# Kernel optimization log

Hardware: AMD Instinct MI355X
Metric: run time of the kernel (lower is better)

The kernel has to match this reference:

```python
import jax, jax.numpy as jnp
import numpy as np


def _laplacian_kernel(x, z, bandwidth):
    x_sq = jnp.sum(x * x, axis=-1, keepdims=True)          # [N, 1]
    z_sq = jnp.sum(z * z, axis=-1)[None, :]                # [1, M]
    d2 = x_sq + z_sq - 2.0 * jnp.einsum('nd,md->nm', x, z)  # [N, M]
    d = jnp.sqrt(jnp.maximum(d2, 0.0))
    return jnp.exp(-d / bandwidth)


def setup_inputs() -> dict:
    key = jax.random.key(0)
    k1, k2, k3 = jax.random.split(key, 3)
    N, M, D, Y = 8192, 20000, 1024, 256
    batch = jax.random.normal(k1, (N, D), dtype=jnp.float32)
    centers = jax.random.normal(k2, (M, D), dtype=jnp.float32)
    weight = jax.random.normal(k3, (M, Y), dtype=jnp.float32) * 0.02
    return {"batch": batch, "centers": centers, "weight": weight, "bandwidth": 10}


def reference(batch, centers, weight, bandwidth):
    kmat = _laplacian_kernel(batch, centers, float(bandwidth))  # [N, M]
    pred = kmat @ weight                                        # [N, Y]
    return pred
```

## Files before the change

### kernel.cpp

```cpp
#include <hip/hip_runtime.h>
#include <stdint.h>

#define N_ROWS 8192
#define D_DIM  1024
#define M_CENT 20000
#define M_PAD  20224
#define M_TILES 79
#define Y_DIM  256
#define BM 64
#define BN 256
#define BK 64
#define NCHUNK 16
#define MSPLIT 8
#define TILES_PER_SPLIT 10
#define LDSP_STRIDE 264

#define BUFE 20480
#define ZOFF 4096
#define POFF 20480

typedef __attribute__((ext_vector_type(4))) float  f32x4;
typedef __attribute__((ext_vector_type(8))) __bf16 bf16x8;

__device__ __forceinline__ unsigned short f2bf(float f) {
    union { float f; unsigned u; } v; v.f = f;
    unsigned u = v.u;
    u += 0x7FFFu + ((u >> 16) & 1u);
    return (unsigned short)(u >> 16);
}

__device__ __forceinline__ void gll16(void* lds, const void* g) {
    __builtin_amdgcn_global_load_lds(
        (const __attribute__((address_space(1))) void*)g,
        (__attribute__((address_space(3))) void*)lds, 16, 0, 0);
}

__global__ void cast_rows_kernel(const float* __restrict__ src,
                                 unsigned short* __restrict__ dst,
                                 float* __restrict__ sq, int nrows_valid) {
    int row = blockIdx.x;
    int t = threadIdx.x;
    float s = 0.f;
    if (row < nrows_valid) {
        float4 v = ((const float4*)(src + (size_t)row * D_DIM))[t];
        s = v.x * v.x + v.y * v.y + v.z * v.z + v.w * v.w;
        ushort4 o;
        o.x = f2bf(v.x); o.y = f2bf(v.y); o.z = f2bf(v.z); o.w = f2bf(v.w);
        ((ushort4*)(dst + (size_t)row * D_DIM))[t] = o;
    } else {
        ((ushort4*)(dst + (size_t)row * D_DIM))[t] = make_ushort4(0, 0, 0, 0);
    }
    __shared__ float red[4];
    for (int off = 32; off; off >>= 1) s += __shfl_down(s, off, 64);
    if ((t & 63) == 0) red[t >> 6] = s;
    __syncthreads();
    if (t == 0) sq[row] = red[0] + red[1] + red[2] + red[3];
}

__global__ void cast_wT_kernel(const float* __restrict__ w,
                               unsigned short* __restrict__ wT) {
    __shared__ float tile[32][33];
    int k0 = blockIdx.x * 32;
    int y0 = blockIdx.y * 32;
    int tx = threadIdx.x & 31;
    int ty = threadIdx.x >> 5;
    #pragma unroll
    for (int i = 0; i < 4; ++i) {
        int k = k0 + ty + i * 8;
        float v = (k < M_CENT) ? w[(size_t)k * Y_DIM + y0 + tx] : 0.f;
        tile[tx][ty + i * 8] = v;
    }
    __syncthreads();
    #pragma unroll
    for (int i = 0; i < 4; ++i) {
        int yl = ty + i * 8;
        wT[(size_t)(y0 + yl) * M_PAD + k0 + tx] = f2bf(tile[yl][tx]);
    }
}


#define STAGE(PAR, M0, KBASE) do {                                            \
    _Pragma("unroll")                                                         \
    for (int i_ = 0; i_ < 2; ++i_) {                   \
        int lin_ = t + i_ * 256;                                              \
        int row_ = lin_ >> 3, c_ = lin_ & 7;                                  \
        gll16(&lds_all[(PAR) * BUFE + lin_ * 8],                              \
              Xb + (size_t)(row0 + row_) * D_DIM + (KBASE) +                  \
                  ((c_ ^ (row_ & 7)) * 8));                                   \
    }                                                                         \
    _Pragma("unroll")                                                         \
    for (int i_ = 0; i_ < 8; ++i_) {                  \
        int lin_ = t + i_ * 256;                                              \
        int row_ = lin_ >> 3, c_ = lin_ & 7;                                  \
        gll16(&lds_all[(PAR) * BUFE + ZOFF + lin_ * 8],                       \
              Zb + (size_t)((M0) + row_) * D_DIM + (KBASE) +                  \
                  ((c_ ^ (row_ & 7)) * 8));                                   \
    } } while (0)

#define CHUNK(PAR, M0N, KBN) do {                                             \
    asm volatile("" ::: "memory");                                            \
    __builtin_amdgcn_s_barrier();                  \
    asm volatile("" ::: "memory");                                            \
    STAGE(PAR ^ 1, M0N, KBN);                                                 \
    __builtin_amdgcn_sched_barrier(0);                                        \
    asm volatile("s_waitcnt vmcnt(10)" ::: "memory");     \
    __builtin_amdgcn_s_barrier();            \
    asm volatile("" ::: "memory");                                            \
    _Pragma("unroll")                                                         \
    for (int kt_ = 0; kt_ < 2; ++kt_) {                                       \
        const int sw_ = ((kt_ * 4 + quad) ^ cx) * 8;                          \
        bf16x8 a_[4], b_[4];                                                  \
        _Pragma("unroll")                                                     \
        for (int it_ = 0; it_ < 4; ++it_)                                     \
            a_[it_] = *(const bf16x8*)&lds_all[(PAR) * BUFE +                 \
                (it_ * 16 + l16) * BK + sw_];                                 \
        _Pragma("unroll")                                                     \
        for (int jt_ = 0; jt_ < 4; ++jt_)                                     \
            b_[jt_] = *(const bf16x8*)&lds_all[(PAR) * BUFE + ZOFF +          \
                (wave * 64 + jt_ * 16 + l16) * BK + sw_];                     \
        __builtin_amdgcn_s_setprio(1);                                        \
        _Pragma("unroll")                                                     \
        for (int it_ = 0; it_ < 4; ++it_)                                     \
            _Pragma("unroll")                                                 \
            for (int jt_ = 0; jt_ < 4; ++jt_)                                 \
                S[it_ * 4 + jt_] = __builtin_amdgcn_mfma_f32_16x16x32_bf16(   \
                    a_[it_], b_[jt_], S[it_ * 4 + jt_], 0, 0, 0);             \
        __builtin_amdgcn_s_setprio(0);                                        \
    } } while (0)

__global__ void __launch_bounds__(256, 2)
fused_kernel(const unsigned short* __restrict__ Xb,
             const unsigned short* __restrict__ Zb,
             const unsigned short* __restrict__ WbT,
             const float* __restrict__ xsq,
             const float* __restrict__ zsq,
             const int* __restrict__ bwp,
             float* __restrict__ out) {
    __shared__ unsigned short lds_all[2 * BUFE];

    const int t    = threadIdx.x;
    const int wave = t >> 6;
    const int lane = t & 63;
    const int quad = lane >> 4;
    const int l16  = lane & 15;
    const int cx   = l16 & 7;

    const int row0 = blockIdx.x * BM;
    const int mt0  = blockIdx.y * TILES_PER_SPLIT;
    int mt_end = mt0 + TILES_PER_SPLIT;
    if (mt_end > M_TILES) mt_end = M_TILES;

    int bwi = *bwp;
    float bw;
    if (bwi > 0 && bwi < 1000000) bw = (float)bwi;
    else { union { int i; float f; } u; u.i = bwi; bw = u.f; }
    const float inv_bw = 1.0f / bw;

    const f32x4 vzero = {0.f, 0.f, 0.f, 0.f};
    f32x4 Oacc[16];
    #pragma unroll
    for (int i = 0; i < 16; ++i) Oacc[i] = vzero;

    STAGE(0, mt0 * BN, 0);
    __builtin_amdgcn_sched_barrier(0);

    for (int mt = mt0; mt < mt_end; ++mt) {
        const int m0 = mt * BN;
        const int m0next = (mt + 1 < mt_end) ? m0 + BN : m0;

        f32x4 S[16];
        #pragma unroll
        for (int i = 0; i < 16; ++i) S[i] = vzero;

        #pragma unroll 1
        for (int kc = 0; kc < NCHUNK; kc += 2) {
            const bool last = (kc + 2 == NCHUNK);
            CHUNK(0, m0, (kc + 1) * BK);
            CHUNK(1, last ? m0next : m0, last ? 0 : (kc + 2) * BK);
        }

        asm volatile("" ::: "memory");
        __builtin_amdgcn_s_barrier();
        asm volatile("" ::: "memory");

        f32x4 xq[4];
        #pragma unroll
        for (int it = 0; it < 4; ++it)
            xq[it] = *(const f32x4*)(xsq + row0 + it * 16 + quad * 4);
        float zq[4];
        #pragma unroll
        for (int jt = 0; jt < 4; ++jt)
            zq[jt] = zsq[m0 + wave * 64 + jt * 16 + l16];

        #pragma unroll
        for (int it = 0; it < 4; ++it) {
            #pragma unroll
            for (int jt = 0; jt < 4; ++jt) {
                f32x4 s4 = S[it * 4 + jt];
                const int col = wave * 64 + jt * 16 + l16;
                #pragma unroll
                for (int r = 0; r < 4; ++r) {
                    const int row = it * 16 + quad * 4 + r;
                    float d2 = xq[it][r] + zq[jt] - 2.0f * s4[r];
                    d2 = fmaxf(d2, 0.f);
                    float d;
                    asm("v_sqrt_f32 %0, %1" : "=v"(d) : "v"(d2));
                    float p = __expf(-d * inv_bw);
                    lds_all[POFF + row * LDSP_STRIDE + col] = f2bf(p);
                }
            }
        }
        asm volatile("s_waitcnt lgkmcnt(0)" ::: "memory");
        __builtin_amdgcn_s_barrier();
        asm volatile("" ::: "memory");

        #pragma unroll
        for (int ks = 0; ks < 8; ++ks) {
            const int koff = ks * 32 + quad * 8;
            bf16x8 a[4], b[4];
            #pragma unroll
            for (int rt = 0; rt < 4; ++rt)
                a[rt] = *(const bf16x8*)&lds_all[POFF +
                    (rt * 16 + l16) * LDSP_STRIDE + koff];
            #pragma unroll
            for (int ct = 0; ct < 4; ++ct) {
                const int y = wave * 64 + ct * 16 + l16;
                b[ct] = *(const bf16x8*)(WbT + (size_t)y * M_PAD + m0 + koff);
            }
            __builtin_amdgcn_s_setprio(1);
            #pragma unroll
            for (int rt = 0; rt < 4; ++rt)
                #pragma unroll
                for (int ct = 0; ct < 4; ++ct)
                    Oacc[rt * 4 + ct] = __builtin_amdgcn_mfma_f32_16x16x32_bf16(
                        a[rt], b[ct], Oacc[rt * 4 + ct], 0, 0, 0);
            __builtin_amdgcn_s_setprio(0);
        }
    }

    asm volatile("s_waitcnt vmcnt(0)" ::: "memory");

    #pragma unroll
    for (int rt = 0; rt < 4; ++rt) {
        #pragma unroll
        for (int ct = 0; ct < 4; ++ct) {
            f32x4 v = Oacc[rt * 4 + ct];
            const int y = wave * 64 + ct * 16 + l16;
            #pragma unroll
            for (int r = 0; r < 4; ++r) {
                const int row = row0 + rt * 16 + quad * 4 + r;
                atomicAdd(&out[(size_t)row * Y_DIM + y], v[r]);
            }
        }
    }
}

extern "C" void kernel_launch(void* const* d_in, const int* in_sizes, int n_in,
                              void* d_out, int out_size, void* d_ws, size_t ws_size,
                              hipStream_t stream) {
    const float* X = (const float*)d_in[0];
    const float* Z = (const float*)d_in[1];
    const float* W = (const float*)d_in[2];
    const int*  bw = (const int*)d_in[3];
    float* out = (float*)d_out;

    char* ws = (char*)d_ws;
    size_t off = 0;
    unsigned short* Xb  = (unsigned short*)(ws + off); off += (size_t)N_ROWS * D_DIM * 2;
    unsigned short* Zb  = (unsigned short*)(ws + off); off += (size_t)M_PAD * D_DIM * 2;
    unsigned short* WbT = (unsigned short*)(ws + off); off += (size_t)Y_DIM * M_PAD * 2;
    float* xsq = (float*)(ws + off); off += (size_t)N_ROWS * 4;
    float* zsq = (float*)(ws + off); off += (size_t)M_PAD * 4;

    hipMemsetAsync(d_out, 0, (size_t)out_size * sizeof(float), stream);
    cast_rows_kernel<<<N_ROWS, 256, 0, stream>>>(X, Xb, xsq, N_ROWS);
    cast_rows_kernel<<<M_PAD, 256, 0, stream>>>(Z, Zb, zsq, M_CENT);
    cast_wT_kernel<<<dim3(M_PAD / 32, Y_DIM / 32), 256, 0, stream>>>(W, WbT);
    fused_kernel<<<dim3(N_ROWS / BM, MSPLIT), 256, 0, stream>>>(
        Xb, Zb, WbT, xsq, zsq, bw, out);
}
```

Baseline: 711.6 us.

## Load center tiles directly into registers and stage only batch rows in LDS

The centers (Z) operand of the distance GEMM is no longer staged through LDS. Each wave now reads its own 64-row slice with per-lane 16-byte global loads straight into registers, since waves never shared those rows. Only the small batch tile is still double-buffered in LDS, which shrinks the shared buffers, and the squared norms are cached in LDS. In exchange, the Z loads are issued in the same chunk that consumes them rather than prefetched, so global latency is more exposed, and the row-strided per-lane loads coalesce less well.

After: 982.9 us. +38.1%, slower.

```diff
diff --git a/kernel.cpp b/kernel.cpp
--- a/kernel.cpp
+++ b/kernel.cpp
@@ -15,9 +15,8 @@
 #define TILES_PER_SPLIT 10
 #define LDSP_STRIDE 264
 
-#define BUFE 20480
-#define ZOFF 4096
-#define POFF 20480
+#define BUFE 4096
+#define POFF 8192
 
 typedef __attribute__((ext_vector_type(4))) float  f32x4;
 typedef __attribute__((ext_vector_type(8))) __bf16 bf16x8;
@@ -79,7 +78,7 @@
 }
 
 
-#define STAGE(PAR, M0, KBASE) do {                                            \
+#define STAGE_X(PAR, KBASE) do {                                              \
     _Pragma("unroll")                                                         \
     for (int i_ = 0; i_ < 2; ++i_) {                   \
         int lin_ = t + i_ * 256;                                              \
@@ -87,44 +86,41 @@
         gll16(&lds_all[(PAR) * BUFE + lin_ * 8],                              \
               Xb + (size_t)(row0 + row_) * D_DIM + (KBASE) +                  \
                   ((c_ ^ (row_ & 7)) * 8));                                   \
-    }                                                                         \
+    } } while (0)
+
+#define CHUNK(PAR, M0, KB, KBN) do {                                          \
+    __builtin_amdgcn_sched_barrier(0);          \
+    bf16x8 b8[8];                                                             \
     _Pragma("unroll")                                                         \
-    for (int i_ = 0; i_ < 8; ++i_) {                  \
-        int lin_ = t + i_ * 256;                                              \
-        int row_ = lin_ >> 3, c_ = lin_ & 7;                                  \
-        gll16(&lds_all[(PAR) * BUFE + ZOFF + lin_ * 8],                       \
-              Zb + (size_t)((M0) + row_) * D_DIM + (KBASE) +                  \
-                  ((c_ ^ (row_ & 7)) * 8));                                   \
-    } } while (0)
-
-#define CHUNK(PAR, M0N, KBN) do {                                             \
+    for (int kt_ = 0; kt_ < 2; ++kt_)                                         \
+        _Pragma("unroll")                                                     \
+        for (int jt_ = 0; jt_ < 4; ++jt_)                                     \
+            b8[kt_ * 4 + jt_] = *(const bf16x8*)(Zb +                         \
+                (size_t)((M0) + wave * 64 + jt_ * 16 + l16) * D_DIM +         \
+                (KB) + kt_ * 32 + quad * 8);                                  \
     asm volatile("" ::: "memory");                                            \
     __builtin_amdgcn_s_barrier();                  \
     asm volatile("" ::: "memory");                                            \
-    STAGE(PAR ^ 1, M0N, KBN);                                                 \
+    STAGE_X(PAR ^ 1, KBN);                                                    \
     __builtin_amdgcn_sched_barrier(0);                                        \
-    asm volatile("s_waitcnt vmcnt(10)" ::: "memory");     \
-    __builtin_amdgcn_s_barrier();            \
+    asm volatile("s_waitcnt vmcnt(10)" ::: "memory");       \
+    __builtin_amdgcn_s_barrier();              \
     asm volatile("" ::: "memory");                                            \
     _Pragma("unroll")                                                         \
     for (int kt_ = 0; kt_ < 2; ++kt_) {                                       \
         const int sw_ = ((kt_ * 4 + quad) ^ cx) * 8;                          \
-        bf16x8 a_[4], b_[4];                                                  \
+        bf16x8 a_[4];                                                         \
         _Pragma("unroll")                                                     \
         for (int it_ = 0; it_ < 4; ++it_)                                     \
             a_[it_] = *(const bf16x8*)&lds_all[(PAR) * BUFE +                 \
                 (it_ * 16 + l16) * BK + sw_];                                 \
-        _Pragma("unroll")                                                     \
-        for (int jt_ = 0; jt_ < 4; ++jt_)                                     \
-            b_[jt_] = *(const bf16x8*)&lds_all[(PAR) * BUFE + ZOFF +          \
-                (wave * 64 + jt_ * 16 + l16) * BK + sw_];                     \
         __builtin_amdgcn_s_setprio(1);                                        \
         _Pragma("unroll")                                                     \
         for (int it_ = 0; it_ < 4; ++it_)                                     \
             _Pragma("unroll")                                                 \
             for (int jt_ = 0; jt_ < 4; ++jt_)                                 \
                 S[it_ * 4 + jt_] = __builtin_amdgcn_mfma_f32_16x16x32_bf16(   \
-                    a_[it_], b_[jt_], S[it_ * 4 + jt_], 0, 0, 0);             \
+                    a_[it_], b8[kt_ * 4 + jt_], S[it_ * 4 + jt_], 0, 0, 0);   \
         __builtin_amdgcn_s_setprio(0);                                        \
     } } while (0)
 
@@ -136,7 +132,9 @@
              const float* __restrict__ zsq,
              const int* __restrict__ bwp,
              float* __restrict__ out) {
-    __shared__ unsigned short lds_all[2 * BUFE];
+    __shared__ unsigned short lds_all[POFF + BM * LDSP_STRIDE];
+    __shared__ float lds_xsq[BM];
+    __shared__ float lds_zsq[BN];
 
     const int t    = threadIdx.x;
     const int wave = t >> 6;
@@ -156,17 +154,21 @@
     else { union { int i; float f; } u; u.i = bwi; bw = u.f; }
     const float inv_bw = 1.0f / bw;
 
+    if (t < BM) lds_xsq[t] = xsq[row0 + t];
+
     const f32x4 vzero = {0.f, 0.f, 0.f, 0.f};
     f32x4 Oacc[16];
     #pragma unroll
     for (int i = 0; i < 16; ++i) Oacc[i] = vzero;
 
-    STAGE(0, mt0 * BN, 0);
+    STAGE_X(0, 0);
     __builtin_amdgcn_sched_barrier(0);
 
     for (int mt = mt0; mt < mt_end; ++mt) {
         const int m0 = mt * BN;
-        const int m0next = (mt + 1 < mt_end) ? m0 + BN : m0;
+
+        lds_zsq[t] = zsq[m0 + t];
+        asm volatile("s_waitcnt lgkmcnt(0)" ::: "memory");
 
         f32x4 S[16];
         #pragma unroll
@@ -175,22 +177,9 @@
         #pragma unroll 1
         for (int kc = 0; kc < NCHUNK; kc += 2) {
             const bool last = (kc + 2 == NCHUNK);
-            CHUNK(0, m0, (kc + 1) * BK);
-            CHUNK(1, last ? m0next : m0, last ? 0 : (kc + 2) * BK);
-        }
-
-        asm volatile("" ::: "memory");
-        __builtin_amdgcn_s_barrier();
-        asm volatile("" ::: "memory");
-
-        f32x4 xq[4];
-        #pragma unroll
-        for (int it = 0; it < 4; ++it)
-            xq[it] = *(const f32x4*)(xsq + row0 + it * 16 + quad * 4);
-        float zq[4];
-        #pragma unroll
-        for (int jt = 0; jt < 4; ++jt)
-            zq[jt] = zsq[m0 + wave * 64 + jt * 16 + l16];
+            CHUNK(0, m0, kc * BK, (kc + 1) * BK);
+            CHUNK(1, m0, (kc + 1) * BK, last ? 0 : (kc + 2) * BK);
+        }
 
         #pragma unroll
         for (int it = 0; it < 4; ++it) {
@@ -198,10 +187,11 @@
             for (int jt = 0; jt < 4; ++jt) {
                 f32x4 s4 = S[it * 4 + jt];
                 const int col = wave * 64 + jt * 16 + l16;
+                const float zq = lds_zsq[col];
                 #pragma unroll
                 for (int r = 0; r < 4; ++r) {
                     const int row = it * 16 + quad * 4 + r;
-                    float d2 = xq[it][r] + zq[jt] - 2.0f * s4[r];
+                    float d2 = lds_xsq[row] + zq - 2.0f * s4[r];
                     d2 = fmaxf(d2, 0.f);
                     float d;
                     asm("v_sqrt_f32 %0, %1" : "=v"(d) : "v"(d2));
```
